# Kernel tuning notes

Measured on AMD Instinct MI355X. Metric: run time of the kernel, lower is better.

Reference implementation:

```python
import jax, jax.numpy as jnp
import numpy as np

B, C, N = 4, 512, 4096
C8 = C // 8


def setup_inputs() -> dict:
    key = jax.random.key(0)
    ks = jax.random.split(key, 7)
    s = 0.02
    return {
        "x": jax.random.normal(ks[0], (B, C, N), dtype=jnp.float32),
        "Wq": jax.random.normal(ks[1], (C8, C), dtype=jnp.float32) * s,
        "bq": jax.random.normal(ks[2], (C8,), dtype=jnp.float32) * s,
        "Wk": jax.random.normal(ks[3], (C8, C), dtype=jnp.float32) * s,
        "bk": jax.random.normal(ks[4], (C8,), dtype=jnp.float32) * s,
        "Wv": jax.random.normal(ks[5], (C, C), dtype=jnp.float32) * s,
        "bv": jax.random.normal(ks[6], (C,), dtype=jnp.float32) * s,
        "gamma": jnp.float32(1.0),
    }


def reference(x, Wq, bq, Wk, bk, Wv, bv, gamma):
    # kernel-size-1 Conv1d == per-position channel linear map
    # x: [B, C, N]
    q = jnp.einsum("bcn,dc->bnd", x, Wq) + bq              # [B, N, C8] (query permuted)
    k = jnp.einsum("bcn,dc->bdn", x, Wk) + bk[None, :, None]  # [B, C8, N]
    v = jnp.einsum("bcn,dc->bdn", x, Wv) + bv[None, :, None]  # [B, C, N]
    qk = jnp.einsum("bnd,bdm->bnm", q, k)                  # [B, Nq, Nk]
    # NOTE: softmax over dim=1 (the QUERY axis), as in the original torch code
    attn = jax.nn.softmax(qk, axis=1)                      # [B, Nq, Nk]
    out_attn = jnp.einsum("bcn,bnm->bcm", v, attn)         # value @ attn, [B, C, N]
    return gamma * out_attn + x
```

## Files before the change

kernel.cpp:

```cpp
#include <hip/hip_runtime.h>
#include <hip/hip_bf16.h>

#define BB 4
#define CC 512
#define NN 4096
#define DD 64

typedef __attribute__((ext_vector_type(8))) short short8;
typedef __attribute__((ext_vector_type(4))) short short4v;
typedef __attribute__((ext_vector_type(4))) float floatx4;

static __device__ __forceinline__ short f2bf(float f) {
  __hip_bfloat16 h = __float2bfloat16(f);
  return *reinterpret_cast<short*>(&h);
}

static __device__ __forceinline__ floatx4 mfma16(short8 a, short8 b, floatx4 c) {
  return __builtin_amdgcn_mfma_f32_16x16x32_bf16(a, b, c, 0, 0, 0);
}

#define GLOAD_LDS16(gp, lp) \
  __builtin_amdgcn_global_load_lds((const __attribute__((address_space(1))) void*)(gp), \
                                   (__attribute__((address_space(3))) void*)(lp), 16, 0, 0)

__global__ void wconv_kernel(const float* __restrict__ Wq, const float* __restrict__ Wk,
                             const float* __restrict__ Wv, short* __restrict__ Wb) {
  int i = blockIdx.x * 256 + threadIdx.x;
  int row = i >> 9, c = i & 511;
  float v;
  if (row < 64)        v = Wq[(row << 9) | c];
  else if (row < 128)  v = Wk[((row - 64) << 9) | c];
  else                 v = Wv[((row - 128) << 9) | c];
  Wb[i] = f2bf(v);
}

__global__ __launch_bounds__(512, 4) void qkv_kernel(
    const float* __restrict__ x, const short* __restrict__ Wb,
    const float* __restrict__ bq, const float* __restrict__ bk,
    const float* __restrict__ bv,
    short* __restrict__ qb, short* __restrict__ kb, short* __restrict__ vb) {
  const int bid = blockIdx.x;
  const int jt = bid % 5;
  const int mt = bid / 5;
  const int b  = mt >> 5;
  const int n0 = (mt & 31) << 7;
  const int tid = threadIdx.x;
  const int w = tid >> 6, lane = tid & 63;
  const int arow = lane & 15, grp = lane >> 4;
  const int wm = w >> 2, wj = w & 3;

  __shared__ short xs[128][72];

  const float* xb = x + (size_t)b * CC * NN;
  const int n4l = (tid & 31) << 2;
  const int c4  = (tid >> 5) << 2;

  floatx4 ld[4];
  #pragma unroll
  for (int i = 0; i < 4; ++i)
    ld[i] = *(const floatx4*)(xb + (size_t)(c4 + i) * NN + n0 + n4l);

  floatx4 acc[4][2];
  #pragma unroll
  for (int i = 0; i < 4; ++i)
    #pragma unroll
    for (int j = 0; j < 2; ++j) acc[i][j] = (floatx4){0.f, 0.f, 0.f, 0.f};

  for (int kk = 0; kk < 8; ++kk) {
    __syncthreads();
    #pragma unroll
    for (int j = 0; j < 4; ++j) {
      short4v pk;
      #pragma unroll
      for (int i = 0; i < 4; ++i) pk[i] = f2bf(ld[i][j]);
      *(short4v*)&xs[n4l + j][c4] = pk;
    }
    __syncthreads();
    if (kk < 7) {
      #pragma unroll
      for (int i = 0; i < 4; ++i)
        ld[i] = *(const floatx4*)(xb + (size_t)((kk + 1) * 64 + c4 + i) * NN + n0 + n4l);
    }
    #pragma unroll
    for (int ks = 0; ks < 2; ++ks) {
      short8 pa[4];
      #pragma unroll
      for (int ms = 0; ms < 4; ++ms)
        pa[ms] = *(const short8*)&xs[wm * 64 + ms * 16 + arow][ks * 32 + grp * 8];
      #pragma unroll
      for (int js = 0; js < 2; ++js) {
        const short* wp = Wb + (size_t)(jt * 128 + wj * 32 + js * 16 + arow) * CC
                        + kk * 64 + ks * 32 + grp * 8;
        short8 bfr = *(const short8*)wp;
        #pragma unroll
        for (int ms = 0; ms < 4; ++ms)
          acc[ms][js] = mfma16(pa[ms], bfr, acc[ms][js]);
      }
    }
  }

  #pragma unroll
  for (int js = 0; js < 2; ++js) {
    int dout = jt * 128 + wj * 32 + js * 16 + arow;
    float bias = (dout < 64) ? bq[dout] : (dout < 128) ? bk[dout - 64] : bv[dout - 128];
    #pragma unroll
    for (int ms = 0; ms < 4; ++ms) {
      int n = n0 + wm * 64 + ms * 16 + grp * 4;
      floatx4 a = acc[ms][js];
      if (dout < 64) {
        #pragma unroll
        for (int r = 0; r < 4; ++r)
          qb[((size_t)b * NN + n + r) * DD + dout] = f2bf(a[r] + bias);
      } else if (dout < 128) {
        #pragma unroll
        for (int r = 0; r < 4; ++r)
          kb[((size_t)b * NN + n + r) * DD + (dout - 64)] = f2bf(a[r] + bias);
      } else {
        short4v pk;
        #pragma unroll
        for (int r = 0; r < 4; ++r) pk[r] = f2bf(a[r] + bias);
        *(short4v*)(vb + ((size_t)b * CC + (dout - 128)) * NN + n) = pk;
      }
    }
  }
}

__global__ __launch_bounds__(512, 4) void attn_kernel(
    const short* __restrict__ qb, const short* __restrict__ kb,
    const short* __restrict__ vb, const float* __restrict__ x,
    const float* __restrict__ gamma, float* __restrict__ out) {
  const int bid = blockIdx.x;
  const int xcd = bid & 7;
  const int b = xcd >> 1, ch = xcd & 1;
  const int m0 = (bid >> 3) << 6;
  const int tid = threadIdx.x;
  const int w = tid >> 6, lane = tid & 63;
  const int arow = lane & 15, grp = lane >> 4;
  const int nsub = w & 3;
  const int mh = w >> 2;
  const int wc = w & 3;

  __shared__ short vbuf[256 * 64];
  __shared__ short pbuf[2][64 * 64];
  __shared__ float dsum[4][64];

  const short* qB = qb + (size_t)b * NN * DD;
  const short* kB = kb + (size_t)b * NN * DD;
  const short* vB = vb + ((size_t)b * CC + ch * 256) * NN;

  const int dma_row = (lane >> 3);
  const int dma_nsw = ((lane & 7) ^ dma_row) << 3;

  short8 afr[2][2];
  #pragma unroll
  for (int h = 0; h < 2; ++h) {
    const short* kr = kB + (size_t)(m0 + mh * 32 + h * 16 + arow) * DD;
    afr[h][0] = *(const short8*)(kr + grp * 8);
    afr[h][1] = *(const short8*)(kr + 32 + grp * 8);
  }

  floatx4 acc[2][4];
  #pragma unroll
  for (int i = 0; i < 2; ++i)
    #pragma unroll
    for (int j = 0; j < 4; ++j) acc[i][j] = (floatx4){0.f, 0.f, 0.f, 0.f};
  float dl[2][4];
  #pragma unroll
  for (int h = 0; h < 2; ++h)
    #pragma unroll
    for (int r = 0; r < 4; ++r) dl[h][r] = 0.f;

  short8 qa0, qa1;
  {
    const short* qr = qB + (size_t)(nsub * 16 + arow) * DD + grp * 8;
    qa0 = *(const short8*)(qr);
    qa1 = *(const short8*)(qr + 32);
  }

  #pragma unroll
  for (int q = 0; q < 4; ++q) {
    int r = w * 32 + q * 8 + dma_row;
    GLOAD_LDS16(vB + (size_t)r * NN + dma_nsw, vbuf + (w * 32 + q * 8) * 64);
  }
  #pragma unroll
  for (int h = 0; h < 2; ++h) {
    floatx4 s4 = (floatx4){0.f, 0.f, 0.f, 0.f};
    s4 = mfma16(afr[h][0], qa0, s4);
    s4 = mfma16(afr[h][1], qa1, s4);
    int mrow = mh * 32 + h * 16 + grp * 4;
    #pragma unroll
    for (int r = 0; r < 4; ++r) {
      float p = __expf(s4[r]);
      dl[h][r] += p;
      int row = mrow + r;
      pbuf[0][row * 64 + ((nsub * 16 + arow) ^ ((row & 7) << 3))] = f2bf(p);
    }
  }
  {
    const short* qr = qB + (size_t)(64 + nsub * 16 + arow) * DD + grp * 8;
    qa0 = *(const short8*)(qr);
    qa1 = *(const short8*)(qr + 32);
  }
  __syncthreads();

  const int vbase0 = (wc * 64 + arow) * 64 + ((grp ^ (arow & 7)) << 3);
  for (int i = 0; i < 64; ++i) {
    {
      short8 pa[2][2];
      #pragma unroll
      for (int ms = 0; ms < 2; ++ms) {
        int row = mh * 32 + ms * 16 + arow;
        #pragma unroll
        for (int ks = 0; ks < 2; ++ks)
          pa[ms][ks] = *(const short8*)&pbuf[i & 1][row * 64 + ((ks * 32 + grp * 8) ^ ((row & 7) << 3))];
      }
      short8 vv0[4], vv1[4];
      #pragma unroll
      for (int cs = 0; cs < 4; ++cs) {
        vv0[cs] = *(const short8*)&vbuf[vbase0 + cs * 16 * 64];
        vv1[cs] = *(const short8*)&vbuf[(vbase0 + cs * 16 * 64) ^ 32];
      }
      __builtin_amdgcn_s_setprio(1);
      #pragma unroll
      for (int cs = 0; cs < 4; ++cs)
        #pragma unroll
        for (int ms = 0; ms < 2; ++ms)
          acc[ms][cs] = mfma16(pa[ms][0], vv0[cs], acc[ms][cs]);
      #pragma unroll
      for (int cs = 0; cs < 4; ++cs)
        #pragma unroll
        for (int ms = 0; ms < 2; ++ms)
          acc[ms][cs] = mfma16(pa[ms][1], vv1[cs], acc[ms][cs]);
      __builtin_amdgcn_s_setprio(0);
    }
    __syncthreads();
    if (i < 63) {
      const int nb1 = (i + 1) << 6;
      #pragma unroll
      for (int q = 0; q < 4; ++q) {
        int r = w * 32 + q * 8 + dma_row;
        GLOAD_LDS16(vB + (size_t)r * NN + nb1 + dma_nsw, vbuf + (w * 32 + q * 8) * 64);
      }
      #pragma unroll
      for (int h = 0; h < 2; ++h) {
        floatx4 s4 = (floatx4){0.f, 0.f, 0.f, 0.f};
        s4 = mfma16(afr[h][0], qa0, s4);
        s4 = mfma16(afr[h][1], qa1, s4);
        int mrow = mh * 32 + h * 16 + grp * 4;
        #pragma unroll
        for (int r = 0; r < 4; ++r) {
          float p = __expf(s4[r]);
          dl[h][r] += p;
          int row = mrow + r;
          pbuf[(i + 1) & 1][row * 64 + ((nsub * 16 + arow) ^ ((row & 7) << 3))] = f2bf(p);
        }
      }
      if (i < 62) {
        const short* qr = qB + (size_t)(nb1 + 64 + nsub * 16 + arow) * DD + grp * 8;
        qa0 = *(const short8*)(qr);
        qa1 = *(const short8*)(qr + 32);
      }
    }
    __syncthreads();
  }

  #pragma unroll
  for (int off = 1; off < 16; off <<= 1)
    #pragma unroll
    for (int h = 0; h < 2; ++h)
      #pragma unroll
      for (int r = 0; r < 4; ++r)
        dl[h][r] += __shfl_xor(dl[h][r], off);
  if (arow == 0) {
    #pragma unroll
    for (int h = 0; h < 2; ++h)
      #pragma unroll
      for (int r = 0; r < 4; ++r)
        dsum[nsub][mh * 32 + h * 16 + grp * 4 + r] = dl[h][r];
  }
  __syncthreads();

  const float g = *gamma;
  #pragma unroll
  for (int ms = 0; ms < 2; ++ms) {
    int ml = mh * 32 + ms * 16 + grp * 4;
    floatx4 linv;
    #pragma unroll
    for (int r = 0; r < 4; ++r) {
      float l = dsum[0][ml + r] + dsum[1][ml + r] + dsum[2][ml + r] + dsum[3][ml + r];
      linv[r] = g / l;
    }
    #pragma unroll
    for (int cs = 0; cs < 4; ++cs) {
      int c = ch * 256 + wc * 64 + cs * 16 + arow;
      const float* xp = x + ((size_t)b * CC + c) * NN + m0 + ml;
      floatx4 xv = *(const floatx4*)xp;
      floatx4 res;
      #pragma unroll
      for (int r = 0; r < 4; ++r) res[r] = acc[ms][cs][r] * linv[r] + xv[r];
      *(floatx4*)(out + ((size_t)b * CC + c) * NN + m0 + ml) = res;
    }
  }
}

extern "C" void kernel_launch(void* const* d_in, const int* in_sizes, int n_in,
                              void* d_out, int out_size, void* d_ws, size_t ws_size,
                              hipStream_t stream) {
  const float* x     = (const float*)d_in[0];
  const float* Wq    = (const float*)d_in[1];
  const float* bq    = (const float*)d_in[2];
  const float* Wk    = (const float*)d_in[3];
  const float* bk    = (const float*)d_in[4];
  const float* Wv    = (const float*)d_in[5];
  const float* bv    = (const float*)d_in[6];
  const float* gamma = (const float*)d_in[7];
  float* out = (float*)d_out;

  char* ws = (char*)d_ws;
  short* qb = (short*)(ws);
  short* kb = (short*)(ws + (2u << 20));
  short* vb = (short*)(ws + (4u << 20));
  short* Wb = (short*)(ws + (21u << 20));

  hipLaunchKernelGGL(wconv_kernel, dim3(1280), dim3(256), 0, stream, Wq, Wk, Wv, Wb);
  hipLaunchKernelGGL(qkv_kernel, dim3(640), dim3(512), 0, stream,
                     x, Wb, bq, bk, bv, qb, kb, vb);
  hipLaunchKernelGGL(attn_kernel, dim3(512), dim3(512), 0, stream,
                     qb, kb, vb, x, gamma, out);
}
```

Before: 382.3 us.

## Pre-transpose x to bf16, retile QKV projection, and double-buffer V in attention

Adds a transpose kernel that writes x as bf16 in [B,N,C] layout into the output buffer as scratch. The QKV kernel then reads MFMA fragments directly from global memory with no LDS staging, each block covering 32 positions and all 640 output rows. The attention kernel now tiles 128 keys by 128 channels per block and double-buffers V so the next tile's DMA and softmax overlap the current MFMA work, with one barrier per iteration instead of two. The cost is an extra launch and a bf16 round trip of x through memory, plus higher LDS use and register pressure in the attention kernel.

```diff
diff --git a/kernel.cpp b/kernel.cpp
--- a/kernel.cpp
+++ b/kernel.cpp
@@ -34,79 +34,86 @@
   Wb[i] = f2bf(v);
 }
 
+__global__ __launch_bounds__(256) void txpose_kernel(const float* __restrict__ x,
+                                                     short* __restrict__ xT) {
+  const int bid = blockIdx.x;
+  const int b  = bid >> 9;
+  const int ct = (bid >> 6) & 7,  c0 = ct << 6;
+  const int nt = bid & 63,        n0 = nt << 6;
+  const int tid = threadIdx.x;
+  const int tn = (tid & 15) << 2;
+  const int tc = tid >> 4;
+
+  __shared__ short t[64][70];
+
+  const float* xb = x + (size_t)b * CC * NN;
+  #pragma unroll
+  for (int i = 0; i < 4; ++i) {
+    int c = tc + i * 16;
+    floatx4 v = *(const floatx4*)(xb + (size_t)(c0 + c) * NN + n0 + tn);
+    short4v pk;
+    #pragma unroll
+    for (int j = 0; j < 4; ++j) pk[j] = f2bf(v[j]);
+    *(short4v*)&t[c][tn] = pk;
+  }
+  __syncthreads();
+  #pragma unroll
+  for (int i = 0; i < 4; ++i) {
+    int n = tc + i * 16;
+    short4v pk;
+    #pragma unroll
+    for (int j = 0; j < 4; ++j) pk[j] = t[tn + j][n];
+    *(short4v*)(xT + ((size_t)b * NN + n0 + n) * CC + c0 + tn) = pk;
+  }
+}
+
 __global__ __launch_bounds__(512, 4) void qkv_kernel(
-    const float* __restrict__ x, const short* __restrict__ Wb,
+    const short* __restrict__ xT, const short* __restrict__ Wb,
     const float* __restrict__ bq, const float* __restrict__ bk,
     const float* __restrict__ bv,
     short* __restrict__ qb, short* __restrict__ kb, short* __restrict__ vb) {
   const int bid = blockIdx.x;
-  const int jt = bid % 5;
-  const int mt = bid / 5;
-  const int b  = mt >> 5;
-  const int n0 = (mt & 31) << 7;
+  const int b  = bid >> 7;
+  const int n0 = (bid & 127) << 5;
   const int tid = threadIdx.x;
   const int w = tid >> 6, lane = tid & 63;
   const int arow = lane & 15, grp = lane >> 4;
-  const int wm = w >> 2, wj = w & 3;
-
-  __shared__ short xs[128][72];
-
-  const float* xb = x + (size_t)b * CC * NN;
-  const int n4l = (tid & 31) << 2;
-  const int c4  = (tid >> 5) << 2;
-
-  floatx4 ld[4];
-  #pragma unroll
-  for (int i = 0; i < 4; ++i)
-    ld[i] = *(const floatx4*)(xb + (size_t)(c4 + i) * NN + n0 + n4l);
-
-  floatx4 acc[4][2];
-  #pragma unroll
-  for (int i = 0; i < 4; ++i)
-    #pragma unroll
-    for (int j = 0; j < 2; ++j) acc[i][j] = (floatx4){0.f, 0.f, 0.f, 0.f};
+
+  floatx4 acc[2][5];
+  #pragma unroll
+  for (int i = 0; i < 2; ++i)
+    #pragma unroll
+    for (int j = 0; j < 5; ++j) acc[i][j] = (floatx4){0.f, 0.f, 0.f, 0.f};
+
+  const short* aB = xT + ((size_t)b * NN + n0) * CC;
+  const short* wB = Wb + (size_t)(w * 80) * CC;
 
   for (int kk = 0; kk < 8; ++kk) {
-    __syncthreads();
-    #pragma unroll
-    for (int j = 0; j < 4; ++j) {
-      short4v pk;
-      #pragma unroll
-      for (int i = 0; i < 4; ++i) pk[i] = f2bf(ld[i][j]);
-      *(short4v*)&xs[n4l + j][c4] = pk;
-    }
-    __syncthreads();
-    if (kk < 7) {
-      #pragma unroll
-      for (int i = 0; i < 4; ++i)
-        ld[i] = *(const floatx4*)(xb + (size_t)((kk + 1) * 64 + c4 + i) * NN + n0 + n4l);
-    }
     #pragma unroll
     for (int ks = 0; ks < 2; ++ks) {
-      short8 pa[4];
-      #pragma unroll
-      for (int ms = 0; ms < 4; ++ms)
-        pa[ms] = *(const short8*)&xs[wm * 64 + ms * 16 + arow][ks * 32 + grp * 8];
-      #pragma unroll
-      for (int js = 0; js < 2; ++js) {
-        const short* wp = Wb + (size_t)(jt * 128 + wj * 32 + js * 16 + arow) * CC
-                        + kk * 64 + ks * 32 + grp * 8;
-        short8 bfr = *(const short8*)wp;
-        #pragma unroll
-        for (int ms = 0; ms < 4; ++ms)
-          acc[ms][js] = mfma16(pa[ms], bfr, acc[ms][js]);
-      }
-    }
-  }
-
-  #pragma unroll
-  for (int js = 0; js < 2; ++js) {
-    int dout = jt * 128 + wj * 32 + js * 16 + arow;
+      const int ko = kk * 64 + ks * 32 + grp * 8;
+      short8 af[2];
+      #pragma unroll
+      for (int ms = 0; ms < 2; ++ms)
+        af[ms] = *(const short8*)(aB + (size_t)(ms * 16 + arow) * CC + ko);
+      #pragma unroll
+      for (int ds = 0; ds < 5; ++ds) {
+        short8 wf = *(const short8*)(wB + (size_t)(ds * 16 + arow) * CC + ko);
+        #pragma unroll
+        for (int ms = 0; ms < 2; ++ms)
+          acc[ms][ds] = mfma16(af[ms], wf, acc[ms][ds]);
+      }
+    }
+  }
+
+  #pragma unroll
+  for (int ds = 0; ds < 5; ++ds) {
+    int dout = w * 80 + ds * 16 + arow;
     float bias = (dout < 64) ? bq[dout] : (dout < 128) ? bk[dout - 64] : bv[dout - 128];
     #pragma unroll
-    for (int ms = 0; ms < 4; ++ms) {
-      int n = n0 + wm * 64 + ms * 16 + grp * 4;
-      floatx4 a = acc[ms][js];
+    for (int ms = 0; ms < 2; ++ms) {
+      int n = n0 + ms * 16 + grp * 4;
+      floatx4 a = acc[ms][ds];
       if (dout < 64) {
         #pragma unroll
         for (int r = 0; r < 4; ++r)
@@ -131,8 +138,10 @@
     const float* __restrict__ gamma, float* __restrict__ out) {
   const int bid = blockIdx.x;
   const int xcd = bid & 7;
-  const int b = xcd >> 1, ch = xcd & 1;
-  const int m0 = (bid >> 3) << 6;
+  const int slot = bid >> 3;
+  const int slice = xcd + 8 * (slot & 1);
+  const int b = slice >> 2, ch = slice & 3;
+  const int m0 = (slot >> 1) << 7;
   const int tid = threadIdx.x;
   const int w = tid >> 6, lane = tid & 63;
   const int arow = lane & 15, grp = lane >> 4;
@@ -140,33 +149,33 @@
   const int mh = w >> 2;
   const int wc = w & 3;
 
-  __shared__ short vbuf[256 * 64];
-  __shared__ short pbuf[2][64 * 64];
-  __shared__ float dsum[4][64];
+  __shared__ short vbuf[2][128 * 64];
+  __shared__ short pbuf[2][128 * 64];
+  __shared__ float dsum[4][128];
 
   const short* qB = qb + (size_t)b * NN * DD;
   const short* kB = kb + (size_t)b * NN * DD;
-  const short* vB = vb + ((size_t)b * CC + ch * 256) * NN;
-
-  const int dma_row = (lane >> 3);
+  const short* vB = vb + ((size_t)b * CC + ch * 128) * NN;
+
+  const int dma_row = lane >> 3;
   const int dma_nsw = ((lane & 7) ^ dma_row) << 3;
 
-  short8 afr[2][2];
-  #pragma unroll
-  for (int h = 0; h < 2; ++h) {
-    const short* kr = kB + (size_t)(m0 + mh * 32 + h * 16 + arow) * DD;
+  short8 afr[4][2];
+  #pragma unroll
+  for (int h = 0; h < 4; ++h) {
+    const short* kr = kB + (size_t)(m0 + mh * 64 + h * 16 + arow) * DD;
     afr[h][0] = *(const short8*)(kr + grp * 8);
     afr[h][1] = *(const short8*)(kr + 32 + grp * 8);
   }
 
-  floatx4 acc[2][4];
-  #pragma unroll
-  for (int i = 0; i < 2; ++i)
-    #pragma unroll
-    for (int j = 0; j < 4; ++j) acc[i][j] = (floatx4){0.f, 0.f, 0.f, 0.f};
-  float dl[2][4];
-  #pragma unroll
-  for (int h = 0; h < 2; ++h)
+  floatx4 acc[4][2];
+  #pragma unroll
+  for (int i = 0; i < 4; ++i)
+    #pragma unroll
+    for (int j = 0; j < 2; ++j) acc[i][j] = (floatx4){0.f, 0.f, 0.f, 0.f};
+  float dl[4][4];
+  #pragma unroll
+  for (int h = 0; h < 4; ++h)
     #pragma unroll
     for (int r = 0; r < 4; ++r) dl[h][r] = 0.f;
 
@@ -178,16 +187,15 @@
   }
 
   #pragma unroll
-  for (int q = 0; q < 4; ++q) {
-    int r = w * 32 + q * 8 + dma_row;
-    GLOAD_LDS16(vB + (size_t)r * NN + dma_nsw, vbuf + (w * 32 + q * 8) * 64);
-  }
-  #pragma unroll
-  for (int h = 0; h < 2; ++h) {
+  for (int q2 = 0; q2 < 2; ++q2)
+    GLOAD_LDS16(vB + (size_t)(w * 16 + q2 * 8 + dma_row) * NN + dma_nsw,
+                &vbuf[0][(w * 16 + q2 * 8) * 64]);
+  #pragma unroll
+  for (int h = 0; h < 4; ++h) {
     floatx4 s4 = (floatx4){0.f, 0.f, 0.f, 0.f};
     s4 = mfma16(afr[h][0], qa0, s4);
     s4 = mfma16(afr[h][1], qa1, s4);
-    int mrow = mh * 32 + h * 16 + grp * 4;
+    int mrow = mh * 64 + h * 16 + grp * 4;
     #pragma unroll
     for (int r = 0; r < 4; ++r) {
       float p = __expf(s4[r]);
@@ -203,87 +211,84 @@
   }
   __syncthreads();
 
-  const int vbase0 = (wc * 64 + arow) * 64 + ((grp ^ (arow & 7)) << 3);
   for (int i = 0; i < 64; ++i) {
-    {
-      short8 pa[2][2];
-      #pragma unroll
-      for (int ms = 0; ms < 2; ++ms) {
-        int row = mh * 32 + ms * 16 + arow;
-        #pragma unroll
-        for (int ks = 0; ks < 2; ++ks)
-          pa[ms][ks] = *(const short8*)&pbuf[i & 1][row * 64 + ((ks * 32 + grp * 8) ^ ((row & 7) << 3))];
-      }
-      short8 vv0[4], vv1[4];
-      #pragma unroll
-      for (int cs = 0; cs < 4; ++cs) {
-        vv0[cs] = *(const short8*)&vbuf[vbase0 + cs * 16 * 64];
-        vv1[cs] = *(const short8*)&vbuf[(vbase0 + cs * 16 * 64) ^ 32];
-      }
-      __builtin_amdgcn_s_setprio(1);
-      #pragma unroll
-      for (int cs = 0; cs < 4; ++cs)
-        #pragma unroll
-        for (int ms = 0; ms < 2; ++ms)
-          acc[ms][cs] = mfma16(pa[ms][0], vv0[cs], acc[ms][cs]);
-      #pragma unroll
-      for (int cs = 0; cs < 4; ++cs)
-        #pragma unroll
-        for (int ms = 0; ms < 2; ++ms)
-          acc[ms][cs] = mfma16(pa[ms][1], vv1[cs], acc[ms][cs]);
-      __builtin_amdgcn_s_setprio(0);
-    }
-    __syncthreads();
+    const int cur = i & 1, nxt = cur ^ 1;
     if (i < 63) {
       const int nb1 = (i + 1) << 6;
       #pragma unroll
-      for (int q = 0; q < 4; ++q) {
-        int r = w * 32 + q * 8 + dma_row;
-        GLOAD_LDS16(vB + (size_t)r * NN + nb1 + dma_nsw, vbuf + (w * 32 + q * 8) * 64);
-      }
-      #pragma unroll
-      for (int h = 0; h < 2; ++h) {
+      for (int q2 = 0; q2 < 2; ++q2)
+        GLOAD_LDS16(vB + (size_t)(w * 16 + q2 * 8 + dma_row) * NN + nb1 + dma_nsw,
+                    &vbuf[nxt][(w * 16 + q2 * 8) * 64]);
+      #pragma unroll
+      for (int h = 0; h < 4; ++h) {
         floatx4 s4 = (floatx4){0.f, 0.f, 0.f, 0.f};
         s4 = mfma16(afr[h][0], qa0, s4);
         s4 = mfma16(afr[h][1], qa1, s4);
-        int mrow = mh * 32 + h * 16 + grp * 4;
+        int mrow = mh * 64 + h * 16 + grp * 4;
         #pragma unroll
         for (int r = 0; r < 4; ++r) {
           float p = __expf(s4[r]);
           dl[h][r] += p;
           int row = mrow + r;
-          pbuf[(i + 1) & 1][row * 64 + ((nsub * 16 + arow) ^ ((row & 7) << 3))] = f2bf(p);
+          pbuf[nxt][row * 64 + ((nsub * 16 + arow) ^ ((row & 7) << 3))] = f2bf(p);
         }
       }
       if (i < 62) {
-        const short* qr = qB + (size_t)(nb1 + 64 + nsub * 16 + arow) * DD + grp * 8;
+        const short* qr = qB + (size_t)(((i + 2) << 6) + nsub * 16 + arow) * DD + grp * 8;
         qa0 = *(const short8*)(qr);
         qa1 = *(const short8*)(qr + 32);
       }
     }
+    {
+      short8 pa[4][2];
+      #pragma unroll
+      for (int ms = 0; ms < 4; ++ms) {
+        int row = mh * 64 + ms * 16 + arow;
+        #pragma unroll
+        for (int ks = 0; ks < 2; ++ks)
+          pa[ms][ks] = *(const short8*)&pbuf[cur][row * 64 +
+                          ((ks * 32 + grp * 8) ^ ((arow & 7) << 3))];
+      }
+      short8 vv[2][2];
+      #pragma unroll
+      for (int cs = 0; cs < 2; ++cs) {
+        int vb0 = (wc * 32 + cs * 16 + arow) * 64 + ((grp ^ (arow & 7)) << 3);
+        vv[cs][0] = *(const short8*)&vbuf[cur][vb0];
+        vv[cs][1] = *(const short8*)&vbuf[cur][vb0 ^ 32];
+      }
+      __builtin_amdgcn_s_setprio(1);
+      #pragma unroll
+      for (int ks = 0; ks < 2; ++ks)
+        #pragma unroll
+        for (int cs = 0; cs < 2; ++cs)
+          #pragma unroll
+          for (int ms = 0; ms < 4; ++ms)
+            acc[ms][cs] = mfma16(pa[ms][ks], vv[cs][ks], acc[ms][cs]);
+      __builtin_amdgcn_s_setprio(0);
+    }
     __syncthreads();
   }
 
   #pragma unroll
   for (int off = 1; off < 16; off <<= 1)
     #pragma unroll
-    for (int h = 0; h < 2; ++h)
+    for (int h = 0; h < 4; ++h)
       #pragma unroll
       for (int r = 0; r < 4; ++r)
         dl[h][r] += __shfl_xor(dl[h][r], off);
   if (arow == 0) {
     #pragma unroll
-    for (int h = 0; h < 2; ++h)
+    for (int h = 0; h < 4; ++h)
       #pragma unroll
       for (int r = 0; r < 4; ++r)
-        dsum[nsub][mh * 32 + h * 16 + grp * 4 + r] = dl[h][r];
+        dsum[nsub][mh * 64 + h * 16 + grp * 4 + r] = dl[h][r];
   }
   __syncthreads();
 
   const float g = *gamma;
   #pragma unroll
-  for (int ms = 0; ms < 2; ++ms) {
-    int ml = mh * 32 + ms * 16 + grp * 4;
+  for (int ms = 0; ms < 4; ++ms) {
+    int ml = mh * 64 + ms * 16 + grp * 4;
     floatx4 linv;
     #pragma unroll
     for (int r = 0; r < 4; ++r) {
@@ -291,8 +296,8 @@
       linv[r] = g / l;
     }
     #pragma unroll
-    for (int cs = 0; cs < 4; ++cs) {
-      int c = ch * 256 + wc * 64 + cs * 16 + arow;
+    for (int cs = 0; cs < 2; ++cs) {
+      int c = ch * 128 + wc * 32 + cs * 16 + arow;
       const float* xp = x + ((size_t)b * CC + c) * NN + m0 + ml;
       floatx4 xv = *(const floatx4*)xp;
       floatx4 res;
@@ -321,10 +326,12 @@
   short* kb = (short*)(ws + (2u << 20));
   short* vb = (short*)(ws + (4u << 20));
   short* Wb = (short*)(ws + (21u << 20));
+  short* xT = (short*)d_out;
 
   hipLaunchKernelGGL(wconv_kernel, dim3(1280), dim3(256), 0, stream, Wq, Wk, Wv, Wb);
-  hipLaunchKernelGGL(qkv_kernel, dim3(640), dim3(512), 0, stream,
-                     x, Wb, bq, bk, bv, qb, kb, vb);
+  hipLaunchKernelGGL(txpose_kernel, dim3(4 * 8 * 64), dim3(256), 0, stream, x, xT);
+  hipLaunchKernelGGL(qkv_kernel, dim3(512), dim3(512), 0, stream,
+                     xT, Wb, bq, bk, bv, qb, kb, vb);
   hipLaunchKernelGGL(attn_kernel, dim3(512), dim3(512), 0, stream,
                      qb, kb, vb, x, gamma, out);
 }
```

Result: slower. 692.0 us (+81.0%).

## Double-buffer V tiles in LDS and drop one barrier per iteration

Applied to the files above, without the earlier changes.

V tiles now live in two LDS buffers, so the load of the next V tile and the next P tile is issued before the MFMA work on the current tile. This removes one __syncthreads per loop iteration and lets the DMA and exp work overlap with the matrix multiplies. Shared memory grows to 80KB in one aliased char array, with dsum reusing the P buffer space. That cuts how many blocks can sit on one CU, but the grid gives only about two blocks per CU anyway.

```diff
diff --git a/kernel.cpp b/kernel.cpp
--- a/kernel.cpp
+++ b/kernel.cpp
@@ -140,15 +140,16 @@
   const int mh = w >> 2;
   const int wc = w & 3;
 
-  __shared__ short vbuf[256 * 64];
-  __shared__ short pbuf[2][64 * 64];
-  __shared__ float dsum[4][64];
+  __shared__ __align__(16) char smem[81920];
+  short* vbufA = (short*)smem;
+  short* pbufA = (short*)(smem + 65536);
+  float* dsum  = (float*)(smem + 65536);
 
   const short* qB = qb + (size_t)b * NN * DD;
   const short* kB = kb + (size_t)b * NN * DD;
   const short* vB = vb + ((size_t)b * CC + ch * 256) * NN;
 
-  const int dma_row = (lane >> 3);
+  const int dma_row = lane >> 3;
   const int dma_nsw = ((lane & 7) ^ dma_row) << 3;
 
   short8 afr[2][2];
@@ -178,10 +179,9 @@
   }
 
   #pragma unroll
-  for (int q = 0; q < 4; ++q) {
-    int r = w * 32 + q * 8 + dma_row;
-    GLOAD_LDS16(vB + (size_t)r * NN + dma_nsw, vbuf + (w * 32 + q * 8) * 64);
-  }
+  for (int q = 0; q < 4; ++q)
+    GLOAD_LDS16(vB + (size_t)(w * 32 + q * 8 + dma_row) * NN + dma_nsw,
+                vbufA + (w * 32 + q * 8) * 64);
   #pragma unroll
   for (int h = 0; h < 2; ++h) {
     floatx4 s4 = (floatx4){0.f, 0.f, 0.f, 0.f};
@@ -193,7 +193,7 @@
       float p = __expf(s4[r]);
       dl[h][r] += p;
       int row = mrow + r;
-      pbuf[0][row * 64 + ((nsub * 16 + arow) ^ ((row & 7) << 3))] = f2bf(p);
+      pbufA[row * 64 + ((nsub * 16 + arow) ^ ((row & 7) << 3))] = f2bf(p);
     }
   }
   {
@@ -203,44 +203,18 @@
   }
   __syncthreads();
 
-  const int vbase0 = (wc * 64 + arow) * 64 + ((grp ^ (arow & 7)) << 3);
   for (int i = 0; i < 64; ++i) {
-    {
-      short8 pa[2][2];
-      #pragma unroll
-      for (int ms = 0; ms < 2; ++ms) {
-        int row = mh * 32 + ms * 16 + arow;
-        #pragma unroll
-        for (int ks = 0; ks < 2; ++ks)
-          pa[ms][ks] = *(const short8*)&pbuf[i & 1][row * 64 + ((ks * 32 + grp * 8) ^ ((row & 7) << 3))];
-      }
-      short8 vv0[4], vv1[4];
-      #pragma unroll
-      for (int cs = 0; cs < 4; ++cs) {
-        vv0[cs] = *(const short8*)&vbuf[vbase0 + cs * 16 * 64];
-        vv1[cs] = *(const short8*)&vbuf[(vbase0 + cs * 16 * 64) ^ 32];
-      }
-      __builtin_amdgcn_s_setprio(1);
-      #pragma unroll
-      for (int cs = 0; cs < 4; ++cs)
-        #pragma unroll
-        for (int ms = 0; ms < 2; ++ms)
-          acc[ms][cs] = mfma16(pa[ms][0], vv0[cs], acc[ms][cs]);
-      #pragma unroll
-      for (int cs = 0; cs < 4; ++cs)
-        #pragma unroll
-        for (int ms = 0; ms < 2; ++ms)
-          acc[ms][cs] = mfma16(pa[ms][1], vv1[cs], acc[ms][cs]);
-      __builtin_amdgcn_s_setprio(0);
-    }
-    __syncthreads();
+    const int cur = i & 1, nxt = cur ^ 1;
+    short* vcur = vbufA + cur * 16384;
+    short* vnxt = vbufA + nxt * 16384;
+    short* pcur = pbufA + cur * 4096;
+    short* pnxt = pbufA + nxt * 4096;
     if (i < 63) {
       const int nb1 = (i + 1) << 6;
       #pragma unroll
-      for (int q = 0; q < 4; ++q) {
-        int r = w * 32 + q * 8 + dma_row;
-        GLOAD_LDS16(vB + (size_t)r * NN + nb1 + dma_nsw, vbuf + (w * 32 + q * 8) * 64);
-      }
+      for (int q = 0; q < 4; ++q)
+        GLOAD_LDS16(vB + (size_t)(w * 32 + q * 8 + dma_row) * NN + nb1 + dma_nsw,
+                    vnxt + (w * 32 + q * 8) * 64);
       #pragma unroll
       for (int h = 0; h < 2; ++h) {
         floatx4 s4 = (floatx4){0.f, 0.f, 0.f, 0.f};
@@ -252,14 +226,41 @@
           float p = __expf(s4[r]);
           dl[h][r] += p;
           int row = mrow + r;
-          pbuf[(i + 1) & 1][row * 64 + ((nsub * 16 + arow) ^ ((row & 7) << 3))] = f2bf(p);
+          pnxt[row * 64 + ((nsub * 16 + arow) ^ ((row & 7) << 3))] = f2bf(p);
         }
       }
       if (i < 62) {
-        const short* qr = qB + (size_t)(nb1 + 64 + nsub * 16 + arow) * DD + grp * 8;
+        const short* qr = qB + (size_t)(((i + 2) << 6) + nsub * 16 + arow) * DD + grp * 8;
         qa0 = *(const short8*)(qr);
         qa1 = *(const short8*)(qr + 32);
       }
+    }
+    {
+      short8 pa[2][2];
+      #pragma unroll
+      for (int ms = 0; ms < 2; ++ms) {
+        int row = mh * 32 + ms * 16 + arow;
+        #pragma unroll
+        for (int ks = 0; ks < 2; ++ks)
+          pa[ms][ks] = *(const short8*)&pcur[row * 64 +
+                          ((ks * 32 + grp * 8) ^ ((row & 7) << 3))];
+      }
+      short8 vv[4][2];
+      #pragma unroll
+      for (int cs = 0; cs < 4; ++cs) {
+        int vb0 = (wc * 64 + cs * 16 + arow) * 64 + ((grp ^ (arow & 7)) << 3);
+        vv[cs][0] = *(const short8*)&vcur[vb0];
+        vv[cs][1] = *(const short8*)&vcur[vb0 ^ 32];
+      }
+      __builtin_amdgcn_s_setprio(1);
+      #pragma unroll
+      for (int ks = 0; ks < 2; ++ks)
+        #pragma unroll
+        for (int cs = 0; cs < 4; ++cs)
+          #pragma unroll
+          for (int ms = 0; ms < 2; ++ms)
+            acc[ms][cs] = mfma16(pa[ms][ks], vv[cs][ks], acc[ms][cs]);
+      __builtin_amdgcn_s_setprio(0);
     }
     __syncthreads();
   }
@@ -276,7 +277,7 @@
     for (int h = 0; h < 2; ++h)
       #pragma unroll
       for (int r = 0; r < 4; ++r)
-        dsum[nsub][mh * 32 + h * 16 + grp * 4 + r] = dl[h][r];
+        dsum[nsub * 64 + mh * 32 + h * 16 + grp * 4 + r] = dl[h][r];
   }
   __syncthreads();
 
@@ -287,7 +288,8 @@
     floatx4 linv;
     #pragma unroll
     for (int r = 0; r < 4; ++r) {
-      float l = dsum[0][ml + r] + dsum[1][ml + r] + dsum[2][ml + r] + dsum[3][ml + r];
+      float l = dsum[0 * 64 + ml + r] + dsum[1 * 64 + ml + r]
+              + dsum[2 * 64 + ml + r] + dsum[3 * 64 + ml + r];
       linv[r] = g / l;
     }
     #pragma unroll
```

Measured after the change: 391.8 us. 1.02x slower.
